# Optimization experiments

Measured on AMD Instinct MI355X. Metric: run time of the kernel, lower is better.

Reference implementation:

```python
import jax, jax.numpy as jnp
import numpy as np

TEMPERATURE = 11.313708498984761  # sqrt(d_k) with d_k=128
RELU15_CAP = 15.0


def setup_inputs() -> dict:
    key = jax.random.key(0)
    kq, kk, kv = jax.random.split(key, 3)
    B, H, S, D = 4, 16, 1024, 128
    q = jax.random.normal(kq, (B, H, S, D), dtype=jnp.float32)
    k = jax.random.normal(kk, (B, H, S, D), dtype=jnp.float32)
    v = jax.random.normal(kv, (B, H, S, D), dtype=jnp.float32)
    mask = jnp.ones((B, 1, S, S), dtype=jnp.int32)  # broadcast over heads
    return {"q": q, "k": k, "v": v, "mask": mask}


def reference(q, k, v, mask):
    # attn = (q / temperature) @ k^T  -> [B,H,Sq,Sk]
    attn = jnp.einsum("bhqd,bhkd->bhqk", q / TEMPERATURE, k)
    # masked_fill(mask == 0, -1e9)
    attn = jnp.where(mask == 0, jnp.float32(-1e9), attn)
    # ReLU15 activation (custom softmax replacement): clamp to [0, 15]
    attn = jnp.clip(attn, 0.0, RELU15_CAP)
    # dropout with p=0.0 is identity (inference reference)
    out = jnp.einsum("bhqk,bhkd->bhqd", attn, v)
    return (out, attn)
```

## Files before the change

kernel.cpp:

```cpp
#include <hip/hip_runtime.h>
#include <stdint.h>

#define B_   4
#define H_   16
#define S_   1024
#define D_   128
#define BM   64
#define BN   32
#define NKT  (S_ / BN)
#define NTHREADS 256

typedef float f32x4 __attribute__((ext_vector_type(4)));
typedef short s16x8 __attribute__((ext_vector_type(8)));
typedef short s16x4 __attribute__((ext_vector_type(4)));

static __device__ __forceinline__ uint16_t f2bf(float f) {
  uint32_t u = __float_as_uint(f);
  u += 0x7FFFu + ((u >> 16) & 1u);
  return (uint16_t)(u >> 16);
}
static __device__ __forceinline__ float bf2f(uint16_t h) {
  return __uint_as_float((uint32_t)h << 16);
}

static __device__ __forceinline__ void gl16(const void* g, void* l) {
  __builtin_amdgcn_global_load_lds(
      (const __attribute__((address_space(1))) unsigned int*)g,
      (__attribute__((address_space(3))) unsigned int*)l, 16, 0, 0);
}

#define WSK_BYTES  16777216
#define WSV_BYTES  16777216
#define WSM_BYTES  524288
#define WS_NEED    (WSK_BYTES + WSV_BYTES + WSM_BYTES)

__global__ __launch_bounds__(256)
void prepass_kernel(const float* __restrict__ k, const float* __restrict__ v,
                    const int* __restrict__ mask,
                    char* __restrict__ wsK, char* __restrict__ wsV,
                    uint32_t* __restrict__ wsM)
{
  int gid = blockIdx.x * 256 + threadIdx.x;
  if (gid < 1048576) {
    int tile = gid >> 9, c = gid & 511;
    int ks = c >> 7, nt = (c >> 6) & 1, lane = c & 63;
    int row = (tile & 31) * 32 + 16 * nt + (lane & 15);
    int col = 32 * ks + 8 * (lane >> 4);
    const float* src = k + ((size_t)(tile >> 5) * S_ + row) * D_ + col;
    f32x4 x0 = *(const f32x4*)src;
    f32x4 x1 = *(const f32x4*)(src + 4);
    s16x8 h;
    h[0]=f2bf(x0[0]); h[1]=f2bf(x0[1]); h[2]=f2bf(x0[2]); h[3]=f2bf(x0[3]);
    h[4]=f2bf(x1[0]); h[5]=f2bf(x1[1]); h[6]=f2bf(x1[2]); h[7]=f2bf(x1[3]);
    *(s16x8*)(wsK + (size_t)gid * 16) = h;
  } else if (gid < 2097152) {
    int gv = gid - 1048576;
    int tile = gv >> 9, c = gv & 511;
    int nt = c >> 6, lane = c & 63;
    int llo = lane & 15, lhi = lane >> 4;
    int d   = 16 * nt + llo;
    const float* src = v + ((size_t)(tile >> 5) * S_ + (tile & 31) * 32 + 4 * lhi) * D_ + d;
    s16x8 h;
    #pragma unroll
    for (int p = 0; p < 8; ++p)
      h[p] = f2bf(src[(size_t)((p & 3) + 16 * (p >> 2)) * D_]);
    *(s16x8*)(wsV + (size_t)gv * 16) = h;
  } else if (gid < 2228224) {
    int gm = gid - 2097152;
    int gro = gm >> 5;
    int w   = gm & 31;
    const int* src = mask + (size_t)gro * S_ + w * 32;
    uint32_t bits = 0;
    #pragma unroll
    for (int i = 0; i < 32; ++i) bits |= (src[i] != 0 ? 1u : 0u) << i;
    wsM[((size_t)(gro >> 10) * 32 + w) * 1024 + (gro & 1023)] = bits;
  }
}

__global__ __launch_bounds__(NTHREADS)
__attribute__((amdgpu_waves_per_eu(4, 4)))
void attn_relu15_main(const float* __restrict__ q,
                      const char* __restrict__ wsK, const char* __restrict__ wsV,
                      const uint32_t* __restrict__ wsM,
                      float* __restrict__ outp, float* __restrict__ attnp)
{
  const int blk = blockIdx.x;
  const int g   = (blk & 7) * 128 + (blk >> 3);
  const int bh  = g >> 4;
  const int qt  = g & 15;
  const int b   = bh >> 4;

  const int tid  = threadIdx.x;
  const int lane = tid & 63;
  const int wq   = tid >> 6;
  const int lhi  = lane >> 4;
  const int llo  = lane & 15;

  __shared__ __align__(16) char smem[37376];
  char* const lK0 = smem;
  char* const lV0 = smem + 16384;
  char* const lS  = smem + 32768 + wq * 1152;

  const float*    qg  = q + (size_t)bh * (S_ * D_) + (size_t)qt * BM * D_;
  const char*     kw  = wsK + (size_t)(bh * 32) * 8192;
  const char*     vw  = wsV + (size_t)(bh * 32) * 8192;
  const uint32_t* mwb = wsM + (size_t)b * 32768 + qt * BM + 16 * wq + llo;
  float*          ag  = attnp + (size_t)bh * S_ * S_ + (size_t)qt * BM * S_;
  float*          og  = outp  + (size_t)bh * (S_ * D_) + (size_t)qt * BM * D_;

  const float invT = 0.08838834764831843f;

  s16x8 qf[4];
  {
    const float* qrow = qg + (size_t)(16 * wq + llo) * D_;
    #pragma unroll
    for (int ks = 0; ks < 4; ++ks) {
      int d0 = 32 * ks + 8 * lhi;
      f32x4 x0 = *(const f32x4*)(qrow + d0);
      f32x4 x1 = *(const f32x4*)(qrow + d0 + 4);
      s16x8 h;
      h[0]=f2bf(x0[0]*invT); h[1]=f2bf(x0[1]*invT); h[2]=f2bf(x0[2]*invT); h[3]=f2bf(x0[3]*invT);
      h[4]=f2bf(x1[0]*invT); h[5]=f2bf(x1[1]*invT); h[6]=f2bf(x1[2]*invT); h[7]=f2bf(x1[3]*invT);
      qf[ks] = h;
    }
  }

  #pragma unroll
  for (int rep = 0; rep < 2; ++rep) {
    gl16(kw + rep * 4096 + tid * 16, lK0 + rep * 4096 + wq * 1024);
    gl16(vw + rep * 4096 + tid * 16, lV0 + rep * 4096 + wq * 1024);
  }
  asm volatile("s_waitcnt vmcnt(0) lgkmcnt(0)" ::: "memory");
  __builtin_amdgcn_s_barrier();
  __builtin_amdgcn_sched_barrier(0);

  f32x4 oacc[8];
  #pragma unroll
  for (int i = 0; i < 8; ++i) oacc[i] = (f32x4){0.f,0.f,0.f,0.f};

  int cur = 0;
  for (int kt = 0; kt < NKT; ++kt) {
    const bool pf = (kt + 1 < NKT);
    char* lKc = lK0 + cur * 8192;
    char* lVc = lV0 + cur * 8192;

    uint32_t mword = mwb[(size_t)kt * 1024];
    __builtin_amdgcn_sched_barrier(0);

    if (pf) {
      const char* kn = kw + (size_t)(kt + 1) * 8192;
      const char* vn = vw + (size_t)(kt + 1) * 8192;
      char* lKn = lK0 + (cur ^ 1) * 8192;
      char* lVn = lV0 + (cur ^ 1) * 8192;
      #pragma unroll
      for (int rep = 0; rep < 2; ++rep) {
        gl16(kn + rep * 4096 + tid * 16, lKn + rep * 4096 + wq * 1024);
        gl16(vn + rep * 4096 + tid * 16, lVn + rep * 4096 + wq * 1024);
      }
    }
    __builtin_amdgcn_sched_barrier(0);

    f32x4 sacc[2];
    sacc[0] = (f32x4){0.f,0.f,0.f,0.f}; sacc[1] = sacc[0];
    #pragma unroll
    for (int ks = 0; ks < 4; ++ks) {
      s16x8 bfr[2];
      #pragma unroll
      for (int nt = 0; nt < 2; ++nt)
        bfr[nt] = *(s16x8*)(lKc + (ks * 2 + nt) * 1024 + lane * 16);
      #pragma unroll
      for (int nt = 0; nt < 2; ++nt)
        sacc[nt] = __builtin_amdgcn_mfma_f32_16x16x32_bf16(bfr[nt], qf[ks], sacc[nt], 0, 0, 0);
    }

    s16x8 pa;
    #pragma unroll
    for (int nt = 0; nt < 2; ++nt) {
      #pragma unroll
      for (int j = 0; j < 4; ++j) {
        float val = fminf(fmaxf(sacc[nt][j], 0.f), 15.f);
        if (!((mword >> (16 * nt + 4 * lhi + j)) & 1u)) val = 0.f;
        pa[nt * 4 + j] = (short)f2bf(val);
      }
      s16x4 h4 = { pa[nt*4], pa[nt*4+1], pa[nt*4+2], pa[nt*4+3] };
      *(s16x4*)(lS + llo * 72 + nt * 32 + lhi * 8) = h4;
    }

    #pragma unroll
    for (int nt = 0; nt < 8; ++nt) {
      s16x8 vb = *(s16x8*)(lVc + nt * 1024 + lane * 16);
      oacc[nt] = __builtin_amdgcn_mfma_f32_16x16x32_bf16(pa, vb, oacc[nt], 0, 0, 0);
    }

    #pragma unroll
    for (int p = 0; p < 2; ++p) {
      int rq   = lane >> 3;
      int part = lane & 7;
      int r    = 8 * p + rq;
      s16x4 sv = *(s16x4*)(lS + r * 72 + part * 8);
      f32x4 a;
      a[0]=bf2f((uint16_t)sv[0]); a[1]=bf2f((uint16_t)sv[1]);
      a[2]=bf2f((uint16_t)sv[2]); a[3]=bf2f((uint16_t)sv[3]);
      __builtin_nontemporal_store(a,
          (f32x4*)(ag + (size_t)(16 * wq + r) * S_ + kt * BN + part * 4));
    }

    asm volatile("s_waitcnt vmcnt(2) lgkmcnt(0)" ::: "memory");
    __builtin_amdgcn_s_barrier();
    __builtin_amdgcn_sched_barrier(0);
    cur ^= 1;
  }

  #pragma unroll
  for (int nt = 0; nt < 8; ++nt) {
    int n = 16 * nt + llo;
    #pragma unroll
    for (int j = 0; j < 4; ++j) {
      int m = 16 * wq + 4 * lhi + j;
      __builtin_nontemporal_store(oacc[nt][j], og + (size_t)m * D_ + n);
    }
  }
}

#define LDS_BARRIER() do {                                   \
    asm volatile("s_waitcnt lgkmcnt(0)" ::: "memory");       \
    __builtin_amdgcn_s_barrier();                            \
    __builtin_amdgcn_sched_barrier(0);                       \
  } while (0)

__global__ __launch_bounds__(NTHREADS)
__attribute__((amdgpu_waves_per_eu(4, 4)))
void attn_relu15_fallback(const float* __restrict__ q, const float* __restrict__ k,
                          const float* __restrict__ v, const int* __restrict__ mask,
                          float* __restrict__ outp, float* __restrict__ attnp)
{
  const int blk = blockIdx.x;
  const int g   = (blk & 7) * 128 + (blk >> 3);
  const int bh  = g >> 4;
  const int qt  = g & 15;
  const int b   = bh >> 4;
  const int tid  = threadIdx.x;
  const int lane = tid & 63;
  const int wq   = tid >> 6;
  const int lhi  = lane >> 4;
  const int llo  = lane & 15;

  __shared__ __align__(16) char smem[36864];
  char* const lK0 = smem;
  char* const lV0 = smem + 16384;
  char* const lS  = smem + 32768 + wq * 1024;

  const float* qg = q + (size_t)bh * (S_ * D_) + (size_t)qt * 64 * D_;
  const float* kg = k + (size_t)bh * (S_ * D_);
  const float* vg = v + (size_t)bh * (S_ * D_);
  const int*   mg = mask  + (size_t)b * S_ * S_ + (size_t)qt * 64 * S_;
  float*       ag = attnp + (size_t)bh * S_ * S_ + (size_t)qt * 64 * S_;
  float*       og = outp  + (size_t)bh * (S_ * D_) + (size_t)qt * 64 * D_;
  const float invT = 0.08838834764831843f;

  #define K_O(rep)   ((tid + NTHREADS * (rep)) * 8)
  #define K_ROW(o)   ((((o) >> 10) & 1) * 16 + (((o) >> 4) & 15))
  #define K_COL(o)   (((o) >> 11) * 32 + (((o) >> 8) & 3) * 8 + (((o) >> 3) & 1) * 4)

  s16x8 qf[4];
  {
    const float* qrow = qg + (size_t)(16 * wq + llo) * D_;
    #pragma unroll
    for (int ks = 0; ks < 4; ++ks) {
      int d0 = 32 * ks + 8 * lhi;
      f32x4 x0 = *(const f32x4*)(qrow + d0);
      f32x4 x1 = *(const f32x4*)(qrow + d0 + 4);
      s16x8 h;
      h[0]=f2bf(x0[0]*invT); h[1]=f2bf(x0[1]*invT); h[2]=f2bf(x0[2]*invT); h[3]=f2bf(x0[3]*invT);
      h[4]=f2bf(x1[0]*invT); h[5]=f2bf(x1[1]*invT); h[6]=f2bf(x1[2]*invT); h[7]=f2bf(x1[3]*invT);
      qf[ks] = h;
    }
  }
  {
    #pragma unroll
    for (int rep = 0; rep < 4; ++rep) {
      int o = K_O(rep);
      f32x4 x = *(const f32x4*)(kg + K_ROW(o) * D_ + K_COL(o));
      s16x4 h; h[0]=f2bf(x[0]); h[1]=f2bf(x[1]); h[2]=f2bf(x[2]); h[3]=f2bf(x[3]);
      *(s16x4*)(lK0 + o) = h;
    }
    #pragma unroll
    for (int rep = 0; rep < 4; ++rep) {
      int bid = (tid >> 2) + 64 * rep;
      int kb = bid >> 5, db = bid & 31, l2 = lane & 3;
      f32x4 x = *(const f32x4*)(vg + (size_t)(kb * 4 + l2) * D_ + db * 4);
      float v0=x[0], v1=x[1], v2=x[2], v3=x[3], t;
      t=(l2&1)?v0:v1; t=__shfl_xor(t,1); if(l2&1)v0=t; else v1=t;
      t=(l2&1)?v2:v3; t=__shfl_xor(t,1); if(l2&1)v2=t; else v3=t;
      t=(l2&2)?v0:v2; t=__shfl_xor(t,2); if(l2&2)v0=t; else v2=t;
      t=(l2&2)?v1:v3; t=__shfl_xor(t,2); if(l2&2)v1=t; else v3=t;
      int dd = db * 4 + l2;
      s16x4 h; h[0]=f2bf(v0); h[1]=f2bf(v1); h[2]=f2bf(v2); h[3]=f2bf(v3);
      *(s16x4*)(lV0 + (dd >> 4) * 1024 + ((kb >> 1) & 3) * 256
                    + (dd & 15) * 16 + (kb & 1) * 8) = h;
    }
  }
  LDS_BARRIER();

  f32x4 oacc[8];
  #pragma unroll
  for (int i = 0; i < 8; ++i) oacc[i] = (f32x4){0.f,0.f,0.f,0.f};

  int cur = 0;
  for (int kt = 0; kt < NKT; ++kt) {
    const bool pf = (kt + 1 < NKT);
    char* lKc = lK0 + cur * 8192;
    char* lVc = lV0 + cur * 8192;
    f32x4 kst[4];
    const float* kgt = kg + (size_t)(kt + 1) * BN * D_;
    if (pf) {
      #pragma unroll
      for (int rep = 0; rep < 4; ++rep) {
        int o = K_O(rep);
        kst[rep] = *(const f32x4*)(kgt + K_ROW(o) * D_ + K_COL(o));
      }
    }
    int mreg[8];
    #pragma unroll
    for (int nt = 0; nt < 2; ++nt)
      #pragma unroll
      for (int j = 0; j < 4; ++j)
        mreg[nt * 4 + j] =
          mg[(size_t)(16 * wq + 4 * lhi + j) * S_ + kt * BN + 16 * nt + llo];

    f32x4 sacc[2];
    sacc[0] = (f32x4){0.f,0.f,0.f,0.f}; sacc[1] = sacc[0];
    #pragma unroll
    for (int ks = 0; ks < 4; ++ks) {
      s16x8 bfr[2];
      #pragma unroll
      for (int nt = 0; nt < 2; ++nt)
        bfr[nt] = *(s16x8*)(lKc + (ks * 2 + nt) * 1024 + lane * 16);
      #pragma unroll
      for (int nt = 0; nt < 2; ++nt)
        sacc[nt] = __builtin_amdgcn_mfma_f32_16x16x32_bf16(qf[ks], bfr[nt], sacc[nt], 0, 0, 0);
    }

    f32x4 vst[4];
    const float* vgt = vg + (size_t)(kt + 1) * BN * D_;
    if (pf) {
      char* lKn = lK0 + (cur ^ 1) * 8192;
      #pragma unroll
      for (int rep = 0; rep < 4; ++rep) {
        f32x4 x = kst[rep];
        s16x4 h; h[0]=f2bf(x[0]); h[1]=f2bf(x[1]); h[2]=f2bf(x[2]); h[3]=f2bf(x[3]);
        *(s16x4*)(lKn + K_O(rep)) = h;
      }
      #pragma unroll
      for (int rep = 0; rep < 4; ++rep) {
        int bid = (tid >> 2) + 64 * rep;
        int kb = bid >> 5, db = bid & 31, l2 = lane & 3;
        vst[rep] = *(const f32x4*)(vgt + (size_t)(kb * 4 + l2) * D_ + db * 4);
      }
    }

    #pragma unroll
    for (int nt = 0; nt < 2; ++nt) {
      char* sb = lS + (2 * nt + (llo >> 3)) * 256 + (llo & 7) * 2;
      #pragma unroll
      for (int j = 0; j < 4; ++j) {
        float val = fminf(fmaxf(sacc[nt][j], 0.f), 15.f);
        if (mreg[nt * 4 + j] == 0) val = 0.f;
        *(uint16_t*)(sb + (4 * lhi + j) * 16) = f2bf(val);
      }
    }
    {
      s16x8 saf = *(s16x8*)(lS + lane * 16);
      #pragma unroll
      for (int nt = 0; nt < 8; ++nt) {
        s16x8 vb = *(s16x8*)(lVc + nt * 1024 + lane * 16);
        oacc[nt] = __builtin_amdgcn_mfma_f32_16x16x32_bf16(saf, vb, oacc[nt], 0, 0, 0);
      }
    }
    #pragma unroll
    for (int p = 0; p < 2; ++p) {
      int r  = 16 * wq + p * 8 + (lane >> 3);
      int cb = lane & 7;
      s16x4 sv = *(s16x4*)(lS + (cb >> 1) * 256 + ((r & 15) * 16) + (cb & 1) * 8);
      f32x4 a;
      a[0]=bf2f((uint16_t)sv[0]); a[1]=bf2f((uint16_t)sv[1]);
      a[2]=bf2f((uint16_t)sv[2]); a[3]=bf2f((uint16_t)sv[3]);
      __builtin_nontemporal_store(a, (f32x4*)(ag + (size_t)r * S_ + kt * BN + cb * 4));
    }
    if (pf) {
      char* lVn = lV0 + (cur ^ 1) * 8192;
      #pragma unroll
      for (int rep = 0; rep < 4; ++rep) {
        int bid = (tid >> 2) + 64 * rep;
        int kb = bid >> 5, db = bid & 31, l2 = lane & 3;
        f32x4 x = vst[rep];
        float v0=x[0], v1=x[1], v2=x[2], v3=x[3], t;
        t=(l2&1)?v0:v1; t=__shfl_xor(t,1); if(l2&1)v0=t; else v1=t;
        t=(l2&1)?v2:v3; t=__shfl_xor(t,1); if(l2&1)v2=t; else v3=t;
        t=(l2&2)?v0:v2; t=__shfl_xor(t,2); if(l2&2)v0=t; else v2=t;
        t=(l2&2)?v1:v3; t=__shfl_xor(t,2); if(l2&2)v1=t; else v3=t;
        int dd = db * 4 + l2;
        s16x4 h; h[0]=f2bf(v0); h[1]=f2bf(v1); h[2]=f2bf(v2); h[3]=f2bf(v3);
        *(s16x4*)(lVn + (dd >> 4) * 1024 + ((kb >> 1) & 3) * 256
                      + (dd & 15) * 16 + (kb & 1) * 8) = h;
      }
    }
    LDS_BARRIER();
    cur ^= 1;
  }
  #pragma unroll
  for (int nt = 0; nt < 8; ++nt) {
    int n = 16 * nt + llo;
    #pragma unroll
    for (int j = 0; j < 4; ++j) {
      int m = 16 * wq + 4 * lhi + j;
      __builtin_nontemporal_store(oacc[nt][j], og + (size_t)m * D_ + n);
    }
  }
}

extern "C" void kernel_launch(void* const* d_in, const int* in_sizes, int n_in,
                              void* d_out, int out_size, void* d_ws, size_t ws_size,
                              hipStream_t stream) {
  const float* q    = (const float*)d_in[0];
  const float* k    = (const float*)d_in[1];
  const float* v    = (const float*)d_in[2];
  const int*   mask = (const int*)d_in[3];
  float* outp  = (float*)d_out;
  float* attnp = outp + (size_t)B_ * H_ * S_ * D_;

  if (ws_size >= (size_t)WS_NEED && d_ws != nullptr) {
    char*     wsK = (char*)d_ws;
    char*     wsV = wsK + WSK_BYTES;
    uint32_t* wsM = (uint32_t*)(wsK + WSK_BYTES + WSV_BYTES);
    prepass_kernel<<<8704, 256, 0, stream>>>(k, v, mask, wsK, wsV, wsM);
    attn_relu15_main<<<dim3(B_ * H_ * (S_ / BM)), NTHREADS, 0, stream>>>(
        q, wsK, wsV, wsM, outp, attnp);
  } else {
    attn_relu15_fallback<<<dim3(B_ * H_ * (S_ / 64)), NTHREADS, 0, stream>>>(
        q, k, v, mask, outp, attnp);
  }
}
```

Before: 104.6 us.

## Store attn directly from MFMA regs, vectorize mask loads and stage output via LDS

New measurement: 113.8 us. +8.9%, slower.

```diff
diff --git a/kernel.cpp b/kernel.cpp
--- a/kernel.cpp
+++ b/kernel.cpp
@@ -13,6 +13,7 @@
 typedef float f32x4 __attribute__((ext_vector_type(4)));
 typedef short s16x8 __attribute__((ext_vector_type(8)));
 typedef short s16x4 __attribute__((ext_vector_type(4)));
+typedef int   i32x4 __attribute__((ext_vector_type(4)));
 
 static __device__ __forceinline__ uint16_t f2bf(float f) {
   uint32_t u = __float_as_uint(f);
@@ -73,7 +74,7 @@
     uint32_t bits = 0;
     #pragma unroll
     for (int i = 0; i < 32; ++i) bits |= (src[i] != 0 ? 1u : 0u) << i;
-    wsM[((size_t)(gro >> 10) * 32 + w) * 1024 + (gro & 1023)] = bits;
+    wsM[(size_t)gro * 32 + w] = bits;
   }
 }
 
@@ -96,17 +97,16 @@
   const int lhi  = lane >> 4;
   const int llo  = lane & 15;
 
-  __shared__ __align__(16) char smem[37376];
+  __shared__ __align__(16) char smem[32768];
   char* const lK0 = smem;
   char* const lV0 = smem + 16384;
-  char* const lS  = smem + 32768 + wq * 1152;
-
-  const float*    qg  = q + (size_t)bh * (S_ * D_) + (size_t)qt * BM * D_;
-  const char*     kw  = wsK + (size_t)(bh * 32) * 8192;
-  const char*     vw  = wsV + (size_t)(bh * 32) * 8192;
-  const uint32_t* mwb = wsM + (size_t)b * 32768 + qt * BM + 16 * wq + llo;
-  float*          ag  = attnp + (size_t)bh * S_ * S_ + (size_t)qt * BM * S_;
-  float*          og  = outp  + (size_t)bh * (S_ * D_) + (size_t)qt * BM * D_;
+
+  const float*    qg   = q + (size_t)bh * (S_ * D_) + (size_t)qt * BM * D_;
+  const char*     kw   = wsK + (size_t)(bh * 32) * 8192;
+  const char*     vw   = wsV + (size_t)(bh * 32) * 8192;
+  const uint32_t* mrow = wsM + (size_t)(b * 1024 + qt * BM + 16 * wq + llo) * 32;
+  float*          ag   = attnp + (size_t)bh * S_ * S_ + (size_t)qt * BM * S_;
+  float*          og   = outp  + (size_t)bh * (S_ * D_) + (size_t)qt * BM * D_;
 
   const float invT = 0.08838834764831843f;
 
@@ -125,6 +125,7 @@
     }
   }
 
+  i32x4 mqA = *(const i32x4*)(mrow);
   #pragma unroll
   for (int rep = 0; rep < 2; ++rep) {
     gl16(kw + rep * 4096 + tid * 16, lK0 + rep * 4096 + wq * 1024);
@@ -138,86 +139,83 @@
   #pragma unroll
   for (int i = 0; i < 8; ++i) oacc[i] = (f32x4){0.f,0.f,0.f,0.f};
 
-  int cur = 0;
-  for (int kt = 0; kt < NKT; ++kt) {
-    const bool pf = (kt + 1 < NKT);
-    char* lKc = lK0 + cur * 8192;
-    char* lVc = lV0 + cur * 8192;
-
-    uint32_t mword = mwb[(size_t)kt * 1024];
-    __builtin_amdgcn_sched_barrier(0);
-
-    if (pf) {
-      const char* kn = kw + (size_t)(kt + 1) * 8192;
-      const char* vn = vw + (size_t)(kt + 1) * 8192;
-      char* lKn = lK0 + (cur ^ 1) * 8192;
-      char* lVn = lV0 + (cur ^ 1) * 8192;
-      #pragma unroll
-      for (int rep = 0; rep < 2; ++rep) {
-        gl16(kn + rep * 4096 + tid * 16, lKn + rep * 4096 + wq * 1024);
-        gl16(vn + rep * 4096 + tid * 16, lVn + rep * 4096 + wq * 1024);
-      }
-    }
-    __builtin_amdgcn_sched_barrier(0);
-
-    f32x4 sacc[2];
-    sacc[0] = (f32x4){0.f,0.f,0.f,0.f}; sacc[1] = sacc[0];
-    #pragma unroll
-    for (int ks = 0; ks < 4; ++ks) {
-      s16x8 bfr[2];
-      #pragma unroll
-      for (int nt = 0; nt < 2; ++nt)
-        bfr[nt] = *(s16x8*)(lKc + (ks * 2 + nt) * 1024 + lane * 16);
-      #pragma unroll
-      for (int nt = 0; nt < 2; ++nt)
-        sacc[nt] = __builtin_amdgcn_mfma_f32_16x16x32_bf16(bfr[nt], qf[ks], sacc[nt], 0, 0, 0);
-    }
-
-    s16x8 pa;
-    #pragma unroll
-    for (int nt = 0; nt < 2; ++nt) {
-      #pragma unroll
-      for (int j = 0; j < 4; ++j) {
-        float val = fminf(fmaxf(sacc[nt][j], 0.f), 15.f);
-        if (!((mword >> (16 * nt + 4 * lhi + j)) & 1u)) val = 0.f;
-        pa[nt * 4 + j] = (short)f2bf(val);
-      }
-      s16x4 h4 = { pa[nt*4], pa[nt*4+1], pa[nt*4+2], pa[nt*4+3] };
-      *(s16x4*)(lS + llo * 72 + nt * 32 + lhi * 8) = h4;
-    }
-
-    #pragma unroll
-    for (int nt = 0; nt < 8; ++nt) {
-      s16x8 vb = *(s16x8*)(lVc + nt * 1024 + lane * 16);
-      oacc[nt] = __builtin_amdgcn_mfma_f32_16x16x32_bf16(pa, vb, oacc[nt], 0, 0, 0);
-    }
-
-    #pragma unroll
-    for (int p = 0; p < 2; ++p) {
-      int rq   = lane >> 3;
-      int part = lane & 7;
-      int r    = 8 * p + rq;
-      s16x4 sv = *(s16x4*)(lS + r * 72 + part * 8);
-      f32x4 a;
-      a[0]=bf2f((uint16_t)sv[0]); a[1]=bf2f((uint16_t)sv[1]);
-      a[2]=bf2f((uint16_t)sv[2]); a[3]=bf2f((uint16_t)sv[3]);
-      __builtin_nontemporal_store(a,
-          (f32x4*)(ag + (size_t)(16 * wq + r) * S_ + kt * BN + part * 4));
-    }
-
-    asm volatile("s_waitcnt vmcnt(2) lgkmcnt(0)" ::: "memory");
-    __builtin_amdgcn_s_barrier();
-    __builtin_amdgcn_sched_barrier(0);
-    cur ^= 1;
-  }
-
-  #pragma unroll
-  for (int nt = 0; nt < 8; ++nt) {
-    int n = 16 * nt + llo;
-    #pragma unroll
-    for (int j = 0; j < 4; ++j) {
-      int m = 16 * wq + 4 * lhi + j;
-      __builtin_nontemporal_store(oacc[nt][j], og + (size_t)m * D_ + n);
+  for (int grp = 0; grp < 8; ++grp) {
+    i32x4 mqB = mqA;
+    if (grp < 7) mqB = *(const i32x4*)(mrow + 4 * (grp + 1));
+
+    #pragma unroll
+    for (int u = 0; u < 4; ++u) {
+      const int kt = grp * 4 + u;
+      char* lKc = lK0 + (u & 1) * 8192;
+      char* lVc = lV0 + (u & 1) * 8192;
+
+      if (kt + 1 < NKT) {
+        const char* kn = kw + (size_t)(kt + 1) * 8192;
+        const char* vn = vw + (size_t)(kt + 1) * 8192;
+        char* lKn = lK0 + ((u + 1) & 1) * 8192;
+        char* lVn = lV0 + ((u + 1) & 1) * 8192;
+        #pragma unroll
+        for (int rep = 0; rep < 2; ++rep) {
+          gl16(kn + rep * 4096 + tid * 16, lKn + rep * 4096 + wq * 1024);
+          gl16(vn + rep * 4096 + tid * 16, lVn + rep * 4096 + wq * 1024);
+        }
+      }
+      __builtin_amdgcn_sched_barrier(0);
+
+      f32x4 sacc[2];
+      sacc[0] = (f32x4){0.f,0.f,0.f,0.f}; sacc[1] = sacc[0];
+      #pragma unroll
+      for (int ks = 0; ks < 4; ++ks) {
+        s16x8 bfr[2];
+        #pragma unroll
+        for (int nt = 0; nt < 2; ++nt)
+          bfr[nt] = *(s16x8*)(lKc + (ks * 2 + nt) * 1024 + lane * 16);
+        #pragma unroll
+        for (int nt = 0; nt < 2; ++nt)
+          sacc[nt] = __builtin_amdgcn_mfma_f32_16x16x32_bf16(bfr[nt], qf[ks], sacc[nt], 0, 0, 0);
+      }
+
+      const uint32_t mword = (uint32_t)mqA[u];
+      s16x8 pa;
+      #pragma unroll
+      for (int nt = 0; nt < 2; ++nt) {
+        f32x4 a;
+        #pragma unroll
+        for (int j = 0; j < 4; ++j) {
+          float val = fminf(fmaxf(sacc[nt][j], 0.f), 15.f);
+          if (!((mword >> (16 * nt + 4 * lhi + j)) & 1u)) val = 0.f;
+          a[j] = val;
+          pa[nt * 4 + j] = (short)f2bf(val);
+        }
+        __builtin_nontemporal_store(a,
+            (f32x4*)(ag + (size_t)(16 * wq + llo) * S_ + kt * BN + 16 * nt + 4 * lhi));
+      }
+
+      #pragma unroll
+      for (int nt = 0; nt < 8; ++nt) {
+        s16x8 vb = *(s16x8*)(lVc + nt * 1024 + lane * 16);
+        oacc[nt] = __builtin_amdgcn_mfma_f32_16x16x32_bf16(pa, vb, oacc[nt], 0, 0, 0);
+      }
+
+      asm volatile("s_waitcnt vmcnt(2) lgkmcnt(0)" ::: "memory");
+      __builtin_amdgcn_s_barrier();
+      __builtin_amdgcn_sched_barrier(0);
+    }
+    if (grp < 7) mqA = mqB;
+  }
+
+  {
+    char* lO = smem + wq * 8192;
+    #pragma unroll
+    for (int nt = 0; nt < 8; ++nt)
+      #pragma unroll
+      for (int j = 0; j < 4; ++j)
+        *(float*)(lO + (4 * lhi + j) * 512 + (16 * nt + llo) * 4) = oacc[nt][j];
+    #pragma unroll
+    for (int p = 0; p < 8; ++p) {
+      int f = p * 1024 + lane * 16;
+      f32x4 x = *(f32x4*)(lO + f);
+      __builtin_nontemporal_store(x, (f32x4*)(og + (size_t)(16 * wq) * D_ + (f >> 2)));
     }
   }
 }
```
